# Optimization experiments

Hardware: AMD Instinct MI355X
Metric: run time of the kernel (lower is better)

## Reference

```python
import math
import jax, jax.numpy as jnp
import numpy as np

B, N, HID, NH = 4, 1024, 1024, 16
DH = HID // NH
MLP = int(HID * 4.0)


def _ndense(x, w):
    # NormalizedDense: row-normalize kernel (axis=1 for 2D), alpha=sqrt(w[0].size)=sqrt(out),
    # then divide by sqrt(fan_in).
    norm = jnp.linalg.norm(w, axis=1, keepdims=True)
    alpha = jnp.sqrt(jnp.asarray(w.shape[1], x.dtype))
    wn = w / (norm * alpha + 1e-4)
    wn = wn / jnp.sqrt(jnp.asarray(w.shape[0], x.dtype))
    return x @ wn


def mp_silu(x):
    return jax.nn.silu(x) / 0.596


def pixel_norm(x, eps=1e-4):
    return x * jax.lax.rsqrt(jnp.mean(x * x, axis=-1, keepdims=True) + eps)


def mp_add(a, b, t=0.3):
    return ((1 - t) * a + t * b) / math.sqrt((1 - t) ** 2 + t ** 2)


def setup_inputs() -> dict:
    key = jax.random.key(0)
    ks = jax.random.split(key, 9)
    std = 0.02
    return {
        "x": jax.random.normal(ks[0], (B, N, HID), jnp.float32),
        "c": jax.random.normal(ks[1], (B, HID), jnp.float32),
        "w_cond": std * jax.random.normal(ks[2], (HID, 2 * HID), jnp.float32),
        "w_qkv": std * jax.random.normal(ks[3], (HID, 3 * HID), jnp.float32),
        "w_out": std * jax.random.normal(ks[4], (HID, HID), jnp.float32),
        "w_mlp1": std * jax.random.normal(ks[5], (HID, MLP), jnp.float32),
        "w_mlp2": std * jax.random.normal(ks[6], (MLP, HID), jnp.float32),
        "attn_gain": 0.1 * jax.random.normal(ks[7], (), jnp.float32),
        "mlp_gain": 0.1 * jax.random.normal(ks[8], (), jnp.float32),
    }


def reference(x, c, w_cond, w_qkv, w_out, w_mlp1, w_mlp2, attn_gain, mlp_gain):
    # conditioning -> gain/shift
    cc = mp_silu(c)
    cc = _ndense(cc, w_cond)                       # [B, 2H]
    gain, shift = jnp.split(cc, 2, axis=-1)        # [B, H] each

    # attention branch
    x_cond = pixel_norm(x) * (1 + gain[:, None]) + shift[:, None]
    qkv = _ndense(x_cond, w_qkv)                   # [B, N, 3H]
    q, k, v = jnp.split(qkv, 3, axis=-1)
    q, k, v = pixel_norm(q), pixel_norm(k), pixel_norm(v)

    def split_heads(t):
        return t.reshape(B, N, NH, DH).transpose(0, 2, 1, 3)  # [B, NH, N, DH]

    q, k, v = split_heads(q), split_heads(k), split_heads(v)
    q = q / jnp.sqrt(jnp.sum(q * q, axis=-1, keepdims=True) + 1e-6)
    k = k / jnp.sqrt(jnp.sum(k * k, axis=-1, keepdims=True) + 1e-6)

    attn = jnp.einsum('bhnd,bhmd->bhnm', q, k) / math.sqrt(DH)
    attn = jax.nn.softmax(attn, axis=-1)
    x_attn = jnp.einsum('bhnm,bhmd->bhnd', attn, v)
    x_attn = x_attn.transpose(0, 2, 1, 3).reshape(B, N, HID)
    x_attn = pixel_norm(_ndense(x_attn, w_out)) * jnp.exp(attn_gain)
    x = mp_add(x, x_attn, t=0.3)

    # MLP branch
    x_cond = pixel_norm(x) * (1 + gain[:, None]) + shift[:, None]
    h = mp_silu(pixel_norm(_ndense(x_cond, w_mlp1)))
    x_mlp = pixel_norm(_ndense(h, w_mlp2)) * jnp.exp(mlp_gain)
    x = mp_add(x, x_mlp, t=0.3)
    return x
```

## Files before the change

### kernel.cpp

```cpp
#include <hip/hip_runtime.h>

typedef __bf16 bf16_t;
typedef __attribute__((ext_vector_type(8))) __bf16 bh8;
typedef __attribute__((ext_vector_type(4))) __bf16 bh4;
typedef __attribute__((ext_vector_type(4))) float f32x4;

#define DEV static __device__ __forceinline__

typedef __attribute__((address_space(3))) void lds_void;
typedef const __attribute__((address_space(1))) void glb_void;

DEV void async16(const bf16_t* g, bf16_t* l) {
  __builtin_amdgcn_global_load_lds((glb_void*)g, (lds_void*)l, 16, 0, 0);
}

#define GBAR() asm volatile("s_barrier" ::: "memory")
#define VMW(n) asm volatile("s_waitcnt vmcnt(" #n ")" ::: "memory")

DEV f32x4 mfma16(bh8 a, bh8 b, f32x4 c) {
  return __builtin_amdgcn_mfma_f32_16x16x32_bf16(a, b, c, 0, 0, 0);
}

DEV const bf16_t* lds7(const bf16_t* base, int row, int c) {
  return base + row * 64 + ((c ^ (row & 7)) << 3);
}
DEV bf16_t* ldsP(bf16_t* base, int row, int c) {
  int m = (row & 7) ^ ((row >> 3) & 1);
  return base + row * 64 + ((c ^ m) << 3);
}

DEV float wave_sum(float v) {
#pragma unroll
  for (int m = 32; m > 0; m >>= 1) v += __shfl_xor(v, m, 64);
  return v;
}

DEV float block_sum(float v, float* sbuf) {
  v = wave_sum(v);
  int wid = threadIdx.x >> 6;
  if ((threadIdx.x & 63) == 0) sbuf[wid] = v;
  __syncthreads();
  float r = sbuf[0] + sbuf[1] + sbuf[2] + sbuf[3];
  __syncthreads();
  return r;
}

__global__ void k_wnorm_all(const float* __restrict__ w_cond, const float* __restrict__ w_qkv,
                            const float* __restrict__ w_out, const float* __restrict__ w_mlp1,
                            const float* __restrict__ w_mlp2, float* __restrict__ s) {
  __shared__ float sbuf[4];
  int id = blockIdx.x;
  const float* W; int N, K, row;
  if (id < 1024)      { W = w_cond; N = 2048; K = 1024; row = id; }
  else if (id < 2048) { W = w_qkv;  N = 3072; K = 1024; row = id - 1024; }
  else if (id < 3072) { W = w_out;  N = 1024; K = 1024; row = id - 2048; }
  else if (id < 4096) { W = w_mlp1; N = 4096; K = 1024; row = id - 3072; }
  else                { W = w_mlp2; N = 1024; K = 4096; row = id - 4096; }
  const float4* wr = (const float4*)(W + (size_t)row * N);
  float acc = 0.f;
  for (int i = threadIdx.x; i < (N >> 2); i += 256) {
    float4 w = wr[i];
    acc += w.x*w.x + w.y*w.y + w.z*w.z + w.w*w.w;
  }
  float tot = block_sum(acc, sbuf);
  if (threadIdx.x == 0) {
    float norm = sqrtf(tot);
    s[id] = 1.0f / ((norm * sqrtf((float)N) + 1e-4f) * sqrtf((float)K));
  }
}

__global__ void k_wtrans_all(const float* __restrict__ w_cond, const float* __restrict__ w_qkv,
                             const float* __restrict__ w_out, const float* __restrict__ w_mlp1,
                             const float* __restrict__ w_mlp2, const float* __restrict__ sall,
                             bf16_t* __restrict__ wt_cond, bf16_t* __restrict__ wt_qkv,
                             bf16_t* __restrict__ wt_out, bf16_t* __restrict__ wt_mlp1,
                             bf16_t* __restrict__ wt_mlp2) {
  __shared__ float tile[64][65];
  int id = blockIdx.x;
  const float* W; const float* s; bf16_t* Wt; int K, N, n0, k0;
  if (id < 512)       { W=w_cond; s=sall;      Wt=wt_cond; K=1024; N=2048; int l=id;      n0=(l&31)*64; k0=(l>>5)*64; }
  else if (id < 1280) { W=w_qkv;  s=sall+1024; Wt=wt_qkv;  K=1024; N=3072; int l=id-512;  n0=(l%48)*64; k0=(l/48)*64; }
  else if (id < 1536) { W=w_out;  s=sall+2048; Wt=wt_out;  K=1024; N=1024; int l=id-1280; n0=(l&15)*64; k0=(l>>4)*64; }
  else if (id < 2560) { W=w_mlp1; s=sall+3072; Wt=wt_mlp1; K=1024; N=4096; int l=id-1536; n0=(l&63)*64; k0=(l>>6)*64; }
  else                { W=w_mlp2; s=sall+4096; Wt=wt_mlp2; K=4096; N=1024; int l=id-2560; n0=(l&15)*64; k0=(l>>4)*64; }
  int t = threadIdx.x;
#pragma unroll
  for (int i = t; i < 1024; i += 256) {
    int r = i >> 4, c4 = (i & 15) << 2;
    float sc = s[k0 + r];
    float4 w = *(const float4*)(W + (size_t)(k0 + r) * N + n0 + c4);
    tile[r][c4 + 0] = w.x * sc;
    tile[r][c4 + 1] = w.y * sc;
    tile[r][c4 + 2] = w.z * sc;
    tile[r][c4 + 3] = w.w * sc;
  }
  __syncthreads();
#pragma unroll
  for (int i = t; i < 1024; i += 256) {
    int rr = i >> 4, cc = (i & 15) << 2;
    bh4 o;
    o[0] = (bf16_t)tile[cc + 0][rr];
    o[1] = (bf16_t)tile[cc + 1][rr];
    o[2] = (bf16_t)tile[cc + 2][rr];
    o[3] = (bf16_t)tile[cc + 3][rr];
    *(bh4*)(Wt + (size_t)(n0 + rr) * K + k0 + cc) = o;
  }
}

__global__ void k_cond(const float* __restrict__ c, const bf16_t* __restrict__ wt,
                       float* __restrict__ gs) {
  __shared__ float cc[4][1024];
  int t = threadIdx.x;
  for (int i = t; i < 4096; i += 256) {
    int b = i >> 10, col = i & 1023;
    float x = c[b * 1024 + col];
    float sig = 1.f / (1.f + __expf(-x));
    cc[b][col] = x * sig * (1.f / 0.596f);
  }
  __syncthreads();
  int wid = t >> 6, lane = t & 63;
  int j = blockIdx.x * 4 + wid;
  const bf16_t* wr = wt + (size_t)j * 1024;
  float acc0 = 0, acc1 = 0, acc2 = 0, acc3 = 0;
  for (int i = lane; i < 1024; i += 64) {
    float w = (float)wr[i];
    acc0 += cc[0][i] * w; acc1 += cc[1][i] * w;
    acc2 += cc[2][i] * w; acc3 += cc[3][i] * w;
  }
  float v0 = wave_sum(acc0), v1 = wave_sum(acc1), v2 = wave_sum(acc2), v3 = wave_sum(acc3);
  if (lane == 0) {
    gs[0 * 2048 + j] = v0; gs[1 * 2048 + j] = v1;
    gs[2 * 2048 + j] = v2; gs[3 * 2048 + j] = v3;
  }
}

__global__ void k_xcond(const float* __restrict__ x, const float* __restrict__ gs,
                        bf16_t* __restrict__ xc) {
  __shared__ float sbuf[4];
  int row = blockIdx.x, b = row >> 10, t = threadIdx.x;
  float4 v = ((const float4*)(x + (size_t)row * 1024))[t];
  float ss = v.x*v.x + v.y*v.y + v.z*v.z + v.w*v.w;
  float tot = block_sum(ss, sbuf);
  float r = rsqrtf(tot * (1.f/1024.f) + 1e-4f);
  float4 g  = ((const float4*)(gs + b * 2048))[t];
  float4 sh = ((const float4*)(gs + b * 2048 + 1024))[t];
  bh4 o;
  o[0] = (bf16_t)(v.x * r * (1.f + g.x) + sh.x);
  o[1] = (bf16_t)(v.y * r * (1.f + g.y) + sh.y);
  o[2] = (bf16_t)(v.z * r * (1.f + g.z) + sh.z);
  o[3] = (bf16_t)(v.w * r * (1.f + g.w) + sh.w);
  *(bh4*)(xc + (size_t)row * 1024 + t * 4) = o;
}

__global__ __launch_bounds__(512, 2) void k_gemm8(const bf16_t* __restrict__ A,
                                                  const bf16_t* __restrict__ Bt,
                                                  bf16_t* __restrict__ C,
                                                  int M, int N, int K, int klen) {
  __shared__ __attribute__((aligned(16))) bf16_t As[2][2][256][32];
  __shared__ __attribute__((aligned(16))) bf16_t Bs[2][2][256][32];
  const int ntn = gridDim.x;
  const unsigned flat = blockIdx.x + ntn * blockIdx.y;
  const unsigned q = (ntn * gridDim.y) >> 3;
  const unsigned wg = (flat & 7) * q + (flat >> 3);
  const int m0 = (int)(wg / (unsigned)ntn) * 256;
  const int n0 = (int)(wg % (unsigned)ntn) * 256;
  const size_t kbeg = (size_t)blockIdx.z * klen;
  C += (size_t)blockIdx.z * M * N;
  const int t = threadIdx.x, lane = t & 63;
  const int wm = (t >> 6) >> 2, wn = (t >> 6) & 3;
  const int l15 = lane & 15, quad = lane >> 4;
  const int q8 = (quad ^ ((l15 >> 2) & 2)) * 8;
  const int rA = wm * 128 + l15;
  const int rB = wn * 64 + l15;
  const int sr = t >> 2;
  const int sc = ((t & 3) << 3) ^ ((t & 32) >> 1);
  const int swv = (t >> 6) * 512;
  const bf16_t* AgS = A + (size_t)(m0 + sr) * K + kbeg + sc;
  const bf16_t* BgS = Bt + (size_t)(n0 + sr) * K + kbeg + sc;
  const size_t rstep = (size_t)128 * K;
  const int NT = klen >> 6;
  f32x4 acc[8][4] = {};

#define STG_A(kt_, h_, bb_) { const bf16_t* g = AgS + (kt_) * 64 + (h_) * 32; \
    bf16_t* l = &As[bb_][h_][0][0] + swv; async16(g, l); async16(g + rstep, l + 4096); }
#define STG_B(kt_, h_, bb_) { const bf16_t* g = BgS + (kt_) * 64 + (h_) * 32; \
    bf16_t* l = &Bs[bb_][h_][0][0] + swv; async16(g, l); async16(g + rstep, l + 4096); }

  STG_B(0, 0, 0); STG_B(0, 1, 0);
  STG_A(0, 0, 0); STG_A(0, 1, 0);
  if (NT > 1) { STG_B(1, 0, 1); STG_B(1, 1, 1); VMW(4); } else { VMW(0); }
  GBAR();

  for (int kt = 0; kt < NT; ++kt) {
    const int bb = kt & 1;
    bh8 a[4][2], b[4][2];
#pragma unroll
    for (int m = 0; m < 4; ++m)
#pragma unroll
      for (int kc = 0; kc < 2; ++kc)
        a[m][kc] = *(const bh8*)&As[bb][kc][rA + m * 16][q8];
#pragma unroll
    for (int n = 0; n < 2; ++n)
#pragma unroll
      for (int kc = 0; kc < 2; ++kc)
        b[n][kc] = *(const bh8*)&Bs[bb][kc][rB + n * 16][q8];
    if (kt + 1 < NT) STG_A(kt + 1, 0, bb ^ 1);
    GBAR();
    __builtin_amdgcn_s_setprio(1);
#pragma unroll
    for (int m = 0; m < 4; ++m)
#pragma unroll
      for (int n = 0; n < 2; ++n)
#pragma unroll
        for (int kc = 0; kc < 2; ++kc)
          acc[m][n] = mfma16(a[m][kc], b[n][kc], acc[m][n]);
    __builtin_amdgcn_s_setprio(0);
    GBAR();
#pragma unroll
    for (int n = 0; n < 2; ++n)
#pragma unroll
      for (int kc = 0; kc < 2; ++kc)
        b[2 + n][kc] = *(const bh8*)&Bs[bb][kc][rB + (2 + n) * 16][q8];
    if (kt + 1 < NT) STG_A(kt + 1, 1, bb ^ 1);
    GBAR();
    __builtin_amdgcn_s_setprio(1);
#pragma unroll
    for (int m = 0; m < 4; ++m)
#pragma unroll
      for (int n = 0; n < 2; ++n)
#pragma unroll
        for (int kc = 0; kc < 2; ++kc)
          acc[m][2 + n] = mfma16(a[m][kc], b[2 + n][kc], acc[m][2 + n]);
    __builtin_amdgcn_s_setprio(0);
    GBAR();
#pragma unroll
    for (int m = 0; m < 4; ++m)
#pragma unroll
      for (int kc = 0; kc < 2; ++kc)
        a[m][kc] = *(const bh8*)&As[bb][kc][rA + 64 + m * 16][q8];
    if (kt + 2 < NT) STG_B(kt + 2, 0, bb);
    GBAR();
    __builtin_amdgcn_s_setprio(1);
#pragma unroll
    for (int m = 0; m < 4; ++m)
#pragma unroll
      for (int n = 0; n < 2; ++n)
#pragma unroll
        for (int kc = 0; kc < 2; ++kc)
          acc[4 + m][n] = mfma16(a[m][kc], b[n][kc], acc[4 + m][n]);
    __builtin_amdgcn_s_setprio(0);
    GBAR();
    if (kt + 2 < NT) STG_B(kt + 2, 1, bb);
    __builtin_amdgcn_s_setprio(1);
#pragma unroll
    for (int m = 0; m < 4; ++m)
#pragma unroll
      for (int n = 0; n < 2; ++n)
#pragma unroll
        for (int kc = 0; kc < 2; ++kc)
          acc[4 + m][2 + n] = mfma16(a[m][kc], b[2 + n][kc], acc[4 + m][2 + n]);
    __builtin_amdgcn_s_setprio(0);
    if (kt + 2 < NT) { VMW(4); } else { VMW(0); }
    GBAR();
  }
#undef STG_A
#undef STG_B

  const int cm = m0 + wm * 128 + quad * 4;
  const int cn = n0 + wn * 64 + l15;
#pragma unroll
  for (int m = 0; m < 8; ++m)
#pragma unroll
    for (int n = 0; n < 4; ++n)
#pragma unroll
      for (int r2 = 0; r2 < 4; ++r2)
        C[(size_t)(cm + m * 16 + r2) * N + cn + n * 16] = (bf16_t)acc[m][n][r2];
}

__global__ __launch_bounds__(256, 2) void k_gemm2ph(const bf16_t* __restrict__ A,
                                                    const bf16_t* __restrict__ Bt,
                                                    bf16_t* __restrict__ C,
                                                    int M, int N, int K) {
  __shared__ __attribute__((aligned(16))) bf16_t As[2][2][128][32];
  __shared__ __attribute__((aligned(16))) bf16_t Bs[2][2][128][32];
  const int ntn = gridDim.x;
  const unsigned flat = blockIdx.x + ntn * blockIdx.y;
  const unsigned q = (ntn * gridDim.y) >> 3;
  const unsigned wg = (flat & 7) * q + (flat >> 3);
  const int m0 = (int)(wg / (unsigned)ntn) * 128;
  const int n0 = (int)(wg % (unsigned)ntn) * 128;
  const int t = threadIdx.x, lane = t & 63;
  const int wm = (t >> 6) >> 1, wn = (t >> 6) & 1;
  const int l15 = lane & 15, quad = lane >> 4;
  const int q8 = (quad ^ ((l15 >> 2) & 2)) * 8;
  const int rA = wm * 64 + l15;
  const int rB = wn * 64 + l15;
  const int sr = t >> 2;
  const int sc = ((t & 3) << 3) ^ ((t & 32) >> 1);
  const int swv = (t >> 6) * 512;
  const bf16_t* AgS = A + (size_t)(m0 + sr) * K + sc;
  const bf16_t* BgS = Bt + (size_t)(n0 + sr) * K + sc;
  const size_t rstep = (size_t)64 * K;
  const int NT = K >> 6;
  f32x4 acc[4][4] = {};

#define STG_A(kt_, h_, bb_) { const bf16_t* g = AgS + (kt_) * 64 + (h_) * 32; \
    bf16_t* l = &As[bb_][h_][0][0] + swv; async16(g, l); async16(g + rstep, l + 2048); }
#define STG_B(kt_, h_, bb_) { const bf16_t* g = BgS + (kt_) * 64 + (h_) * 32; \
    bf16_t* l = &Bs[bb_][h_][0][0] + swv; async16(g, l); async16(g + rstep, l + 2048); }

  STG_B(0, 0, 0); STG_B(0, 1, 0);
  STG_A(0, 0, 0); STG_A(0, 1, 0);
  if (NT > 1) { STG_B(1, 0, 1); STG_B(1, 1, 1); VMW(4); } else { VMW(0); }
  GBAR();

  for (int kt = 0; kt < NT; ++kt) {
    const int bb = kt & 1;
    bh8 a[4][2], b[4][2];
#pragma unroll
    for (int m = 0; m < 4; ++m)
#pragma unroll
      for (int kc = 0; kc < 2; ++kc)
        a[m][kc] = *(const bh8*)&As[bb][kc][rA + m * 16][q8];
#pragma unroll
    for (int n = 0; n < 4; ++n)
#pragma unroll
      for (int kc = 0; kc < 2; ++kc)
        b[n][kc] = *(const bh8*)&Bs[bb][kc][rB + n * 16][q8];
    if (kt + 1 < NT) { STG_A(kt + 1, 0, bb ^ 1); STG_A(kt + 1, 1, bb ^ 1); }
    GBAR();
    __builtin_amdgcn_s_setprio(1);
#pragma unroll
    for (int m = 0; m < 4; ++m)
#pragma unroll
      for (int n = 0; n < 2; ++n)
#pragma unroll
        for (int kc = 0; kc < 2; ++kc)
          acc[m][n] = mfma16(a[m][kc], b[n][kc], acc[m][n]);
    __builtin_amdgcn_s_setprio(0);
    GBAR();
    if (kt + 2 < NT) { STG_B(kt + 2, 0, bb); STG_B(kt + 2, 1, bb); }
    __builtin_amdgcn_s_setprio(1);
#pragma unroll
    for (int m = 0; m < 4; ++m)
#pragma unroll
      for (int n = 0; n < 2; ++n)
#pragma unroll
        for (int kc = 0; kc < 2; ++kc)
          acc[m][2 + n] = mfma16(a[m][kc], b[2 + n][kc], acc[m][2 + n]);
    __builtin_amdgcn_s_setprio(0);
    if (kt + 2 < NT) { VMW(4); } else { VMW(0); }
    GBAR();
  }
#undef STG_A
#undef STG_B

  const int cm = m0 + wm * 64 + quad * 4;
  const int cn = n0 + wn * 64 + l15;
#pragma unroll
  for (int m = 0; m < 4; ++m)
#pragma unroll
    for (int n = 0; n < 4; ++n)
#pragma unroll
      for (int r2 = 0; r2 < 4; ++r2)
        C[(size_t)(cm + m * 16 + r2) * N + cn + n * 16] = (bf16_t)acc[m][n][r2];
}

__global__ void k_qkvnorm(const bf16_t* __restrict__ qkv, bf16_t* __restrict__ qo,
                          bf16_t* __restrict__ ko, float* __restrict__ rsv) {
  __shared__ float sbuf[4];
  const int row = blockIdx.x, b = row >> 10, n = row & 1023, t = threadIdx.x;
  const bf16_t* rp = qkv + (size_t)row * 3072;
  bh4 q4 = *(const bh4*)(rp + t * 4);
  bh4 k4 = *(const bh4*)(rp + 1024 + t * 4);
  bh4 v4 = *(const bh4*)(rp + 2048 + t * 4);
  float4 q = {(float)q4[0], (float)q4[1], (float)q4[2], (float)q4[3]};
  float4 k = {(float)k4[0], (float)k4[1], (float)k4[2], (float)k4[3]};
  float4 v = {(float)v4[0], (float)v4[1], (float)v4[2], (float)v4[3]};
  float sq = q.x*q.x + q.y*q.y + q.z*q.z + q.w*q.w;
  float sk = k.x*k.x + k.y*k.y + k.z*k.z + k.w*k.w;
  float sv = v.x*v.x + v.y*v.y + v.z*v.z + v.w*v.w;
  float tq = block_sum(sq, sbuf);
  float tk = block_sum(sk, sbuf);
  float tv = block_sum(sv, sbuf);
  float rq = rsqrtf(tq * (1.f/1024.f) + 1e-4f);
  float rk = rsqrtf(tk * (1.f/1024.f) + 1e-4f);
  float rv = rsqrtf(tv * (1.f/1024.f) + 1e-4f);
  float hq = sq, hk = sk;
#pragma unroll
  for (int m = 1; m < 16; m <<= 1) { hq += __shfl_xor(hq, m, 64); hk += __shfl_xor(hk, m, 64); }
  float qs = rq * rsqrtf(rq*rq*hq + 1e-6f);
  float ks = rk * rsqrtf(rk*rk*hk + 1e-6f);
  int h = t >> 4, d = (t & 15) * 4;
  size_t base = ((size_t)(b * 16 + h) * 1024 + n) * 64 + d;
  bh4 oq, okk;
  oq[0]=(bf16_t)(q.x*qs); oq[1]=(bf16_t)(q.y*qs); oq[2]=(bf16_t)(q.z*qs); oq[3]=(bf16_t)(q.w*qs);
  okk[0]=(bf16_t)(k.x*ks); okk[1]=(bf16_t)(k.y*ks); okk[2]=(bf16_t)(k.z*ks); okk[3]=(bf16_t)(k.w*ks);
  *(bh4*)(qo + base) = oq;
  *(bh4*)(ko + base) = okk;
  if (t == 0) rsv[row] = rv;
}

__global__ void k_vtrans(const bf16_t* __restrict__ qkv, const float* __restrict__ rsv,
                         bf16_t* __restrict__ vt) {
  __shared__ bf16_t tile[64][72];
  const int n0 = blockIdx.x * 64, bh = blockIdx.y;
  const int b = bh >> 4, h = bh & 15;
  const int t = threadIdx.x;
  const bf16_t* src = qkv + ((size_t)(b * 1024 + n0)) * 3072 + 2048 + h * 64;
#pragma unroll
  for (int i = t; i < 512; i += 256) {
    int r = i >> 3, p = (i & 7) * 8;
    float sc = rsv[b * 1024 + n0 + r];
    bh8 vv = *(const bh8*)(src + (size_t)r * 3072 + p);
    bh8 o8;
#pragma unroll
    for (int j = 0; j < 8; j++) o8[j] = (bf16_t)((float)vv[j] * sc);
    *(bh8*)&tile[r][p] = o8;
  }
  __syncthreads();
  bf16_t* dst = vt + (size_t)bh * 64 * 1024 + n0;
#pragma unroll
  for (int i = t; i < 512; i += 256) {
    int d = i & 63, nch = (i >> 6) * 8;
    bh8 o;
#pragma unroll
    for (int j = 0; j < 8; j++) o[j] = tile[nch + j][d];
    *(bh8*)(dst + (size_t)d * 1024 + nch) = o;
  }
}

__global__ __launch_bounds__(256, 2) void k_attn(const bf16_t* __restrict__ Q,
                                                 const bf16_t* __restrict__ K,
                                                 const bf16_t* __restrict__ Vt_g,
                                                 bf16_t* __restrict__ O) {
  __shared__ __attribute__((aligned(16))) bf16_t Qs[128][64];
  __shared__ __attribute__((aligned(16))) bf16_t Ks[2][64][64];
  __shared__ __attribute__((aligned(16))) bf16_t Vt[2][64][64];
  __shared__ __attribute__((aligned(16))) bf16_t Ps[128][64];
  const unsigned flat = blockIdx.x + 8u * blockIdx.y;
  const int qt = (int)((flat >> 3) & 7);
  const int bh = (int)((flat & 7) * 8 + (flat >> 6));
  const int b = bh >> 4, h = bh & 15;
  const int t = threadIdx.x, lane = t & 63, wid = t >> 6;
  const int l15 = lane & 15, quad = lane >> 4;
  const int strip = wid * 32;
  const int srow = t >> 3;
  const int scol = ((t & 7) ^ (srow & 7)) << 3;
  const int swv = wid * 512;
  const bf16_t* Qg = Q + ((size_t)bh * 1024 + qt * 128) * 64;
  const bf16_t* Kg = K + (size_t)bh * 1024 * 64;
  const bf16_t* Vg = Vt_g + (size_t)bh * 64 * 1024;

#pragma unroll
  for (int c2 = 0; c2 < 4; ++c2)
    async16(Qg + (size_t)(c2 * 32 + srow) * 64 + scol, &Qs[0][0] + c2 * 2048 + swv);
#pragma unroll
  for (int r0 = 0; r0 < 64; r0 += 32) {
    async16(Kg + (size_t)(r0 + srow) * 64 + scol, &Ks[0][0][0] + r0 * 64 + swv);
    async16(Vg + (size_t)(r0 + srow) * 1024 + scol, &Vt[0][0][0] + r0 * 64 + swv);
  }
  VMW(0);
  GBAR();

  f32x4 o[2][4] = {};
  float rs[2][4] = {{}, {}};
  for (int kt = 0; kt < 16; ++kt) {
    const int bb = kt & 1;
    const int kv0 = kt * 64;
    if (kt < 15) {
#pragma unroll
      for (int r0 = 0; r0 < 64; r0 += 32) {
        async16(Kg + (size_t)(kv0 + 64 + r0 + srow) * 64 + scol,
                &Ks[bb ^ 1][0][0] + r0 * 64 + swv);
        async16(Vg + (size_t)(r0 + srow) * 1024 + kv0 + 64 + scol,
                &Vt[bb ^ 1][0][0] + r0 * 64 + swv);
      }
    }
    f32x4 s[2][4] = {};
    bh8 aq[2][2], bk[4][2];
#pragma unroll
    for (int rf = 0; rf < 2; ++rf)
#pragma unroll
      for (int kc = 0; kc < 2; ++kc)
        aq[rf][kc] = *(const bh8*)lds7(&Qs[0][0], strip + rf * 16 + l15, kc * 4 + quad);
#pragma unroll
    for (int j = 0; j < 4; ++j)
#pragma unroll
      for (int kc = 0; kc < 2; ++kc)
        bk[j][kc] = *(const bh8*)lds7(&Ks[bb][0][0], j * 16 + l15, kc * 4 + quad);
    __builtin_amdgcn_s_setprio(1);
#pragma unroll
    for (int rf = 0; rf < 2; ++rf)
#pragma unroll
      for (int j = 0; j < 4; ++j)
#pragma unroll
        for (int kc = 0; kc < 2; ++kc)
          s[rf][j] = mfma16(aq[rf][kc], bk[j][kc], s[rf][j]);
    __builtin_amdgcn_s_setprio(0);
#pragma unroll
    for (int rf = 0; rf < 2; ++rf)
#pragma unroll
      for (int j = 0; j < 4; ++j)
#pragma unroll
        for (int r = 0; r < 4; ++r) {
          float p = __expf(s[rf][j][r] * 0.125f);
          bf16_t pb = (bf16_t)p;
          rs[rf][r] += (float)pb;
          int prow = strip + rf * 16 + quad * 4 + r;
          ldsP(&Ps[0][0], prow, j * 2 + (l15 >> 3))[l15 & 7] = pb;
        }
    bh8 ap[2][2], bv[4][2];
#pragma unroll
    for (int rf = 0; rf < 2; ++rf)
#pragma unroll
      for (int kc = 0; kc < 2; ++kc)
        ap[rf][kc] = *(const bh8*)ldsP(&Ps[0][0], strip + rf * 16 + l15, kc * 4 + quad);
#pragma unroll
    for (int j = 0; j < 4; ++j)
#pragma unroll
      for (int kc = 0; kc < 2; ++kc)
        bv[j][kc] = *(const bh8*)lds7(&Vt[bb][0][0], j * 16 + l15, kc * 4 + quad);
    __builtin_amdgcn_s_setprio(1);
#pragma unroll
    for (int rf = 0; rf < 2; ++rf)
#pragma unroll
      for (int j = 0; j < 4; ++j)
#pragma unroll
        for (int kc = 0; kc < 2; ++kc)
          o[rf][j] = mfma16(ap[rf][kc], bv[j][kc], o[rf][j]);
    __builtin_amdgcn_s_setprio(0);
    if (kt < 15) { VMW(0); GBAR(); }
  }
#pragma unroll
  for (int rf = 0; rf < 2; ++rf)
#pragma unroll
    for (int r = 0; r < 4; ++r) {
      float v = rs[rf][r];
      v += __shfl_xor(v, 1, 64); v += __shfl_xor(v, 2, 64);
      v += __shfl_xor(v, 4, 64); v += __shfl_xor(v, 8, 64);
      float inv = 1.f / v;
      int n = qt * 128 + strip + rf * 16 + quad * 4 + r;
#pragma unroll
      for (int j = 0; j < 4; ++j)
        O[((size_t)b * 1024 + n) * 1024 + h * 64 + j * 16 + l15] = (bf16_t)(o[rf][j][r] * inv);
    }
}

__global__ void k_amerge(const bf16_t* __restrict__ y, const float* __restrict__ x,
                         const float* __restrict__ gs, const float* __restrict__ again,
                         bf16_t* __restrict__ x1, bf16_t* __restrict__ xc2) {
  __shared__ float sbuf[4];
  int row = blockIdx.x, b = row >> 10, t = threadIdx.x;
  bh4 a = *(const bh4*)(y + (size_t)row * 1024 + t * 4);
  float4 yv = {(float)a[0], (float)a[1], (float)a[2], (float)a[3]};
  float4 xv = ((const float4*)(x + (size_t)row * 1024))[t];
  float ss = yv.x*yv.x + yv.y*yv.y + yv.z*yv.z + yv.w*yv.w;
  float tot = block_sum(ss, sbuf);
  float r = rsqrtf(tot * (1.f/1024.f) + 1e-4f);
  float ag = __expf(again[0]);
  const float C1 = 0.7f / 0.76157731059f, C2 = 0.3f / 0.76157731059f;
  float4 xo;
  xo.x = C1 * xv.x + C2 * (yv.x * r * ag);
  xo.y = C1 * xv.y + C2 * (yv.y * r * ag);
  xo.z = C1 * xv.z + C2 * (yv.z * r * ag);
  xo.w = C1 * xv.w + C2 * (yv.w * r * ag);
  bh4 x1o;
  x1o[0] = (bf16_t)xo.x; x1o[1] = (bf16_t)xo.y; x1o[2] = (bf16_t)xo.z; x1o[3] = (bf16_t)xo.w;
  *(bh4*)(x1 + (size_t)row * 1024 + t * 4) = x1o;
  float ss1 = xo.x*xo.x + xo.y*xo.y + xo.z*xo.z + xo.w*xo.w;
  float tot1 = block_sum(ss1, sbuf);
  float r1 = rsqrtf(tot1 * (1.f/1024.f) + 1e-4f);
  float4 g  = ((const float4*)(gs + b * 2048))[t];
  float4 sh = ((const float4*)(gs + b * 2048 + 1024))[t];
  bh4 o;
  o[0] = (bf16_t)(xo.x * r1 * (1.f + g.x) + sh.x);
  o[1] = (bf16_t)(xo.y * r1 * (1.f + g.y) + sh.y);
  o[2] = (bf16_t)(xo.z * r1 * (1.f + g.z) + sh.z);
  o[3] = (bf16_t)(xo.w * r1 * (1.f + g.w) + sh.w);
  *(bh4*)(xc2 + (size_t)row * 1024 + t * 4) = o;
}

__global__ void k_mlpnorm(const bf16_t* __restrict__ hf, bf16_t* __restrict__ hb) {
  __shared__ float sbuf[4];
  int row = blockIdx.x, t = threadIdx.x;
  const bf16_t* rp = hf + (size_t)row * 4096;
  float4 v[4]; float ss = 0.f;
#pragma unroll
  for (int i = 0; i < 4; i++) {
    bh4 bv = *(const bh4*)(rp + (t + 256 * i) * 4);
    v[i].x = (float)bv[0]; v[i].y = (float)bv[1]; v[i].z = (float)bv[2]; v[i].w = (float)bv[3];
    ss += v[i].x*v[i].x + v[i].y*v[i].y + v[i].z*v[i].z + v[i].w*v[i].w;
  }
  float tot = block_sum(ss, sbuf);
  float r = rsqrtf(tot * (1.f/4096.f) + 1e-4f);
#pragma unroll
  for (int i = 0; i < 4; i++) {
    float a[4] = {v[i].x, v[i].y, v[i].z, v[i].w};
    bh4 o;
#pragma unroll
    for (int j = 0; j < 4; j++) {
      float u = a[j] * r;
      float sig = 1.f / (1.f + __expf(-u));
      o[j] = (bf16_t)(u * sig * (1.f / 0.596f));
    }
    *(bh4*)(hb + (size_t)row * 4096 + (t + 256 * i) * 4) = o;
  }
}

__global__ void k_fmerge(const bf16_t* __restrict__ y, const bf16_t* __restrict__ x1,
                         const float* __restrict__ mgain, float* __restrict__ out) {
  __shared__ float sbuf[4];
  int row = blockIdx.x, t = threadIdx.x;
  const size_t PS = (size_t)4096 * 1024;
  float4 yv = {0.f, 0.f, 0.f, 0.f};
#pragma unroll
  for (int p = 0; p < 4; p++) {
    bh4 yp = *(const bh4*)(y + p * PS + (size_t)row * 1024 + t * 4);
    yv.x += (float)yp[0]; yv.y += (float)yp[1]; yv.z += (float)yp[2]; yv.w += (float)yp[3];
  }
  bh4 xb = *(const bh4*)(x1 + (size_t)row * 1024 + t * 4);
  float4 xv = {(float)xb[0], (float)xb[1], (float)xb[2], (float)xb[3]};
  float ss = yv.x*yv.x + yv.y*yv.y + yv.z*yv.z + yv.w*yv.w;
  float tot = block_sum(ss, sbuf);
  float r = rsqrtf(tot * (1.f/1024.f) + 1e-4f);
  float mg = __expf(mgain[0]);
  const float C1 = 0.7f / 0.76157731059f, C2 = 0.3f / 0.76157731059f;
  float4 o;
  o.x = C1 * xv.x + C2 * (yv.x * r * mg);
  o.y = C1 * xv.y + C2 * (yv.y * r * mg);
  o.z = C1 * xv.z + C2 * (yv.z * r * mg);
  o.w = C1 * xv.w + C2 * (yv.w * r * mg);
  ((float4*)(out + (size_t)row * 1024))[t] = o;
}

extern "C" void kernel_launch(void* const* d_in, const int* in_sizes, int n_in,
                              void* d_out, int out_size, void* d_ws, size_t ws_size,
                              hipStream_t stream) {
  const float* x      = (const float*)d_in[0];
  const float* c      = (const float*)d_in[1];
  const float* w_cond = (const float*)d_in[2];
  const float* w_qkv  = (const float*)d_in[3];
  const float* w_out  = (const float*)d_in[4];
  const float* w_mlp1 = (const float*)d_in[5];
  const float* w_mlp2 = (const float*)d_in[6];
  const float* again  = (const float*)d_in[7];
  const float* mgain  = (const float*)d_in[8];
  float* out = (float*)d_out;
  char* ws = (char*)d_ws;

  bf16_t* wt_cond = (bf16_t*)(ws + 0);
  bf16_t* wt_qkv  = (bf16_t*)(ws + 4194304);
  bf16_t* wt_out  = (bf16_t*)(ws + 10485760);
  bf16_t* wt_mlp1 = (bf16_t*)(ws + 12582912);
  bf16_t* wt_mlp2 = (bf16_t*)(ws + 20971520);
  float*  sn      = (float*)(ws + 29360128);
  float*  gs      = (float*)(ws + 29392896);
  bf16_t* xc      = (bf16_t*)(ws + 29425664);
  bf16_t* qh      = (bf16_t*)(ws + 37814272);
  bf16_t* kh      = (bf16_t*)(ws + 46202880);
  float*  rsv     = (float*)(ws + 54591488);
  bf16_t* xattn   = (bf16_t*)(ws + 62980096);
  bf16_t* hb      = (bf16_t*)(ws + 37814272);
  bf16_t* x1      = (bf16_t*)(ws + 71368704);
  bf16_t* vt      = (bf16_t*)(ws + 79757312);
  bf16_t* buf_b   = (bf16_t*)(ws + 88145920);

  k_wnorm_all<<<8192, 256, 0, stream>>>(w_cond, w_qkv, w_out, w_mlp1, w_mlp2, sn);
  k_wtrans_all<<<3584, 256, 0, stream>>>(w_cond, w_qkv, w_out, w_mlp1, w_mlp2, sn,
                                         wt_cond, wt_qkv, wt_out, wt_mlp1, wt_mlp2);

  k_cond<<<512, 256, 0, stream>>>(c, wt_cond, gs);
  k_xcond<<<4096, 256, 0, stream>>>(x, gs, xc);
  k_gemm8<<<dim3(12, 16, 1), 512, 0, stream>>>(xc, wt_qkv, buf_b, 4096, 3072, 1024, 1024);
  k_qkvnorm<<<4096, 256, 0, stream>>>(buf_b, qh, kh, rsv);
  k_vtrans<<<dim3(16, 64), 256, 0, stream>>>(buf_b, rsv, vt);
  k_attn<<<dim3(8, 64), 256, 0, stream>>>(qh, kh, vt, xattn);
  k_gemm2ph<<<dim3(8, 32), 256, 0, stream>>>(xattn, wt_out, buf_b, 4096, 1024, 1024);
  k_amerge<<<4096, 256, 0, stream>>>(buf_b, x, gs, again, x1, xc);
  k_gemm8<<<dim3(16, 16, 1), 512, 0, stream>>>(xc, wt_mlp1, buf_b, 4096, 4096, 1024, 1024);
  k_mlpnorm<<<4096, 256, 0, stream>>>(buf_b, hb);
  k_gemm8<<<dim3(4, 16, 4), 512, 0, stream>>>(hb, wt_mlp2, buf_b, 4096, 1024, 4096, 1024);
  k_fmerge<<<4096, 256, 0, stream>>>(buf_b, x1, mgain, out);
  (void)in_sizes; (void)n_in; (void)out_size; (void)ws_size;
}
```

Measured before the change: 352.9 us.

## Fuse weight row-norm into transpose pass and fold scales into activations

Removes the separate weight-norm kernel, which read every weight matrix a second time. Sum-of-squares is now accumulated with atomics inside the transpose kernel, then finalized by a tiny kernel. The per-row scale is applied to the GEMM input activations (cond, xcond, attention output, amerge, mlpnorm) instead of being baked into the transposed weights. This adds two small launches, atomic traffic and slightly different bf16 rounding.

```diff
diff --git a/kernel.cpp b/kernel.cpp
--- a/kernel.cpp
+++ b/kernel.cpp
@@ -45,54 +45,37 @@
   return r;
 }
 
-__global__ void k_wnorm_all(const float* __restrict__ w_cond, const float* __restrict__ w_qkv,
-                            const float* __restrict__ w_out, const float* __restrict__ w_mlp1,
-                            const float* __restrict__ w_mlp2, float* __restrict__ s) {
-  __shared__ float sbuf[4];
-  int id = blockIdx.x;
-  const float* W; int N, K, row;
-  if (id < 1024)      { W = w_cond; N = 2048; K = 1024; row = id; }
-  else if (id < 2048) { W = w_qkv;  N = 3072; K = 1024; row = id - 1024; }
-  else if (id < 3072) { W = w_out;  N = 1024; K = 1024; row = id - 2048; }
-  else if (id < 4096) { W = w_mlp1; N = 4096; K = 1024; row = id - 3072; }
-  else                { W = w_mlp2; N = 1024; K = 4096; row = id - 4096; }
-  const float4* wr = (const float4*)(W + (size_t)row * N);
-  float acc = 0.f;
-  for (int i = threadIdx.x; i < (N >> 2); i += 256) {
-    float4 w = wr[i];
-    acc += w.x*w.x + w.y*w.y + w.z*w.z + w.w*w.w;
-  }
-  float tot = block_sum(acc, sbuf);
-  if (threadIdx.x == 0) {
-    float norm = sqrtf(tot);
-    s[id] = 1.0f / ((norm * sqrtf((float)N) + 1e-4f) * sqrtf((float)K));
-  }
+__global__ void k_zero(float* __restrict__ p) {
+  p[blockIdx.x * 256 + threadIdx.x] = 0.f;
 }
 
 __global__ void k_wtrans_all(const float* __restrict__ w_cond, const float* __restrict__ w_qkv,
                              const float* __restrict__ w_out, const float* __restrict__ w_mlp1,
-                             const float* __restrict__ w_mlp2, const float* __restrict__ sall,
+                             const float* __restrict__ w_mlp2, float* __restrict__ ssq,
                              bf16_t* __restrict__ wt_cond, bf16_t* __restrict__ wt_qkv,
                              bf16_t* __restrict__ wt_out, bf16_t* __restrict__ wt_mlp1,
                              bf16_t* __restrict__ wt_mlp2) {
   __shared__ float tile[64][65];
   int id = blockIdx.x;
-  const float* W; const float* s; bf16_t* Wt; int K, N, n0, k0;
-  if (id < 512)       { W=w_cond; s=sall;      Wt=wt_cond; K=1024; N=2048; int l=id;      n0=(l&31)*64; k0=(l>>5)*64; }
-  else if (id < 1280) { W=w_qkv;  s=sall+1024; Wt=wt_qkv;  K=1024; N=3072; int l=id-512;  n0=(l%48)*64; k0=(l/48)*64; }
-  else if (id < 1536) { W=w_out;  s=sall+2048; Wt=wt_out;  K=1024; N=1024; int l=id-1280; n0=(l&15)*64; k0=(l>>4)*64; }
-  else if (id < 2560) { W=w_mlp1; s=sall+3072; Wt=wt_mlp1; K=1024; N=4096; int l=id-1536; n0=(l&63)*64; k0=(l>>6)*64; }
-  else                { W=w_mlp2; s=sall+4096; Wt=wt_mlp2; K=4096; N=1024; int l=id-2560; n0=(l&15)*64; k0=(l>>4)*64; }
+  const float* W; bf16_t* Wt; int K, N, n0, k0, sb;
+  if (id < 512)       { W=w_cond; Wt=wt_cond; K=1024; N=2048; sb=0;    int l=id;      n0=(l&31)*64; k0=(l>>5)*64; }
+  else if (id < 1280) { W=w_qkv;  Wt=wt_qkv;  K=1024; N=3072; sb=1024; int l=id-512;  n0=(l%48)*64; k0=(l/48)*64; }
+  else if (id < 1536) { W=w_out;  Wt=wt_out;  K=1024; N=1024; sb=2048; int l=id-1280; n0=(l&15)*64; k0=(l>>4)*64; }
+  else if (id < 2560) { W=w_mlp1; Wt=wt_mlp1; K=1024; N=4096; sb=3072; int l=id-1536; n0=(l&63)*64; k0=(l>>6)*64; }
+  else                { W=w_mlp2; Wt=wt_mlp2; K=4096; N=1024; sb=4096; int l=id-2560; n0=(l&15)*64; k0=(l>>4)*64; }
   int t = threadIdx.x;
 #pragma unroll
   for (int i = t; i < 1024; i += 256) {
     int r = i >> 4, c4 = (i & 15) << 2;
-    float sc = s[k0 + r];
     float4 w = *(const float4*)(W + (size_t)(k0 + r) * N + n0 + c4);
-    tile[r][c4 + 0] = w.x * sc;
-    tile[r][c4 + 1] = w.y * sc;
-    tile[r][c4 + 2] = w.z * sc;
-    tile[r][c4 + 3] = w.w * sc;
+    tile[r][c4 + 0] = w.x;
+    tile[r][c4 + 1] = w.y;
+    tile[r][c4 + 2] = w.z;
+    tile[r][c4 + 3] = w.w;
+    float ss = w.x*w.x + w.y*w.y + w.z*w.z + w.w*w.w;
+#pragma unroll
+    for (int m = 1; m < 16; m <<= 1) ss += __shfl_xor(ss, m, 64);
+    if ((t & 15) == 0) atomicAdd(&ssq[sb + k0 + r], ss);
   }
   __syncthreads();
 #pragma unroll
@@ -107,15 +90,27 @@
   }
 }
 
+__global__ void k_sfin(const float* __restrict__ ssq, float* __restrict__ s) {
+  int id = blockIdx.x * 256 + threadIdx.x;
+  int N, K;
+  if (id < 1024)      { N = 2048; K = 1024; }
+  else if (id < 2048) { N = 3072; K = 1024; }
+  else if (id < 3072) { N = 1024; K = 1024; }
+  else if (id < 4096) { N = 4096; K = 1024; }
+  else                { N = 1024; K = 4096; }
+  float norm = sqrtf(ssq[id]);
+  s[id] = 1.0f / ((norm * sqrtf((float)N) + 1e-4f) * sqrtf((float)K));
+}
+
 __global__ void k_cond(const float* __restrict__ c, const bf16_t* __restrict__ wt,
-                       float* __restrict__ gs) {
+                       const float* __restrict__ sc, float* __restrict__ gs) {
   __shared__ float cc[4][1024];
   int t = threadIdx.x;
   for (int i = t; i < 4096; i += 256) {
     int b = i >> 10, col = i & 1023;
     float x = c[b * 1024 + col];
     float sig = 1.f / (1.f + __expf(-x));
-    cc[b][col] = x * sig * (1.f / 0.596f);
+    cc[b][col] = x * sig * (1.f / 0.596f) * sc[col];
   }
   __syncthreads();
   int wid = t >> 6, lane = t & 63;
@@ -135,7 +130,7 @@
 }
 
 __global__ void k_xcond(const float* __restrict__ x, const float* __restrict__ gs,
-                        bf16_t* __restrict__ xc) {
+                        const float* __restrict__ sq, bf16_t* __restrict__ xc) {
   __shared__ float sbuf[4];
   int row = blockIdx.x, b = row >> 10, t = threadIdx.x;
   float4 v = ((const float4*)(x + (size_t)row * 1024))[t];
@@ -144,11 +139,12 @@
   float r = rsqrtf(tot * (1.f/1024.f) + 1e-4f);
   float4 g  = ((const float4*)(gs + b * 2048))[t];
   float4 sh = ((const float4*)(gs + b * 2048 + 1024))[t];
+  float4 sv = ((const float4*)sq)[t];
   bh4 o;
-  o[0] = (bf16_t)(v.x * r * (1.f + g.x) + sh.x);
-  o[1] = (bf16_t)(v.y * r * (1.f + g.y) + sh.y);
-  o[2] = (bf16_t)(v.z * r * (1.f + g.z) + sh.z);
-  o[3] = (bf16_t)(v.w * r * (1.f + g.w) + sh.w);
+  o[0] = (bf16_t)((v.x * r * (1.f + g.x) + sh.x) * sv.x);
+  o[1] = (bf16_t)((v.y * r * (1.f + g.y) + sh.y) * sv.y);
+  o[2] = (bf16_t)((v.z * r * (1.f + g.z) + sh.z) * sv.z);
+  o[3] = (bf16_t)((v.w * r * (1.f + g.w) + sh.w) * sv.w);
   *(bh4*)(xc + (size_t)row * 1024 + t * 4) = o;
 }
 
@@ -433,6 +429,7 @@
 __global__ __launch_bounds__(256, 2) void k_attn(const bf16_t* __restrict__ Q,
                                                  const bf16_t* __restrict__ K,
                                                  const bf16_t* __restrict__ Vt_g,
+                                                 const float* __restrict__ so,
                                                  bf16_t* __restrict__ O) {
   __shared__ __attribute__((aligned(16))) bf16_t Qs[128][64];
   __shared__ __attribute__((aligned(16))) bf16_t Ks[2][64][64];
@@ -532,6 +529,9 @@
     __builtin_amdgcn_s_setprio(0);
     if (kt < 15) { VMW(0); GBAR(); }
   }
+  float soj[4];
+#pragma unroll
+  for (int j = 0; j < 4; ++j) soj[j] = so[h * 64 + j * 16 + l15];
 #pragma unroll
   for (int rf = 0; rf < 2; ++rf)
 #pragma unroll
@@ -543,12 +543,14 @@
       int n = qt * 128 + strip + rf * 16 + quad * 4 + r;
 #pragma unroll
       for (int j = 0; j < 4; ++j)
-        O[((size_t)b * 1024 + n) * 1024 + h * 64 + j * 16 + l15] = (bf16_t)(o[rf][j][r] * inv);
+        O[((size_t)b * 1024 + n) * 1024 + h * 64 + j * 16 + l15] =
+            (bf16_t)(o[rf][j][r] * inv * soj[j]);
     }
 }
 
 __global__ void k_amerge(const bf16_t* __restrict__ y, const float* __restrict__ x,
                          const float* __restrict__ gs, const float* __restrict__ again,
+                         const float* __restrict__ sm1,
                          bf16_t* __restrict__ x1, bf16_t* __restrict__ xc2) {
   __shared__ float sbuf[4];
   int row = blockIdx.x, b = row >> 10, t = threadIdx.x;
@@ -573,15 +575,17 @@
   float r1 = rsqrtf(tot1 * (1.f/1024.f) + 1e-4f);
   float4 g  = ((const float4*)(gs + b * 2048))[t];
   float4 sh = ((const float4*)(gs + b * 2048 + 1024))[t];
+  float4 sv = ((const float4*)sm1)[t];
   bh4 o;
-  o[0] = (bf16_t)(xo.x * r1 * (1.f + g.x) + sh.x);
-  o[1] = (bf16_t)(xo.y * r1 * (1.f + g.y) + sh.y);
-  o[2] = (bf16_t)(xo.z * r1 * (1.f + g.z) + sh.z);
-  o[3] = (bf16_t)(xo.w * r1 * (1.f + g.w) + sh.w);
+  o[0] = (bf16_t)((xo.x * r1 * (1.f + g.x) + sh.x) * sv.x);
+  o[1] = (bf16_t)((xo.y * r1 * (1.f + g.y) + sh.y) * sv.y);
+  o[2] = (bf16_t)((xo.z * r1 * (1.f + g.z) + sh.z) * sv.z);
+  o[3] = (bf16_t)((xo.w * r1 * (1.f + g.w) + sh.w) * sv.w);
   *(bh4*)(xc2 + (size_t)row * 1024 + t * 4) = o;
 }
 
-__global__ void k_mlpnorm(const bf16_t* __restrict__ hf, bf16_t* __restrict__ hb) {
+__global__ void k_mlpnorm(const bf16_t* __restrict__ hf, const float* __restrict__ sm2,
+                          bf16_t* __restrict__ hb) {
   __shared__ float sbuf[4];
   int row = blockIdx.x, t = threadIdx.x;
   const bf16_t* rp = hf + (size_t)row * 4096;
@@ -597,12 +601,14 @@
 #pragma unroll
   for (int i = 0; i < 4; i++) {
     float a[4] = {v[i].x, v[i].y, v[i].z, v[i].w};
+    float4 s4 = ((const float4*)sm2)[t + 256 * i];
+    float sa[4] = {s4.x, s4.y, s4.z, s4.w};
     bh4 o;
 #pragma unroll
     for (int j = 0; j < 4; j++) {
       float u = a[j] * r;
       float sig = 1.f / (1.f + __expf(-u));
-      o[j] = (bf16_t)(u * sig * (1.f / 0.596f));
+      o[j] = (bf16_t)(u * sig * (1.f / 0.596f) * sa[j]);
     }
     *(bh4*)(hb + (size_t)row * 4096 + (t + 256 * i) * 4) = o;
   }
@@ -665,21 +671,23 @@
   bf16_t* x1      = (bf16_t*)(ws + 71368704);
   bf16_t* vt      = (bf16_t*)(ws + 79757312);
   bf16_t* buf_b   = (bf16_t*)(ws + 88145920);
-
-  k_wnorm_all<<<8192, 256, 0, stream>>>(w_cond, w_qkv, w_out, w_mlp1, w_mlp2, sn);
-  k_wtrans_all<<<3584, 256, 0, stream>>>(w_cond, w_qkv, w_out, w_mlp1, w_mlp2, sn,
+  float*  ssq     = gs;
+
+  k_zero<<<32, 256, 0, stream>>>(ssq);
+  k_wtrans_all<<<3584, 256, 0, stream>>>(w_cond, w_qkv, w_out, w_mlp1, w_mlp2, ssq,
                                          wt_cond, wt_qkv, wt_out, wt_mlp1, wt_mlp2);
-
-  k_cond<<<512, 256, 0, stream>>>(c, wt_cond, gs);
-  k_xcond<<<4096, 256, 0, stream>>>(x, gs, xc);
+  k_sfin<<<32, 256, 0, stream>>>(ssq, sn);
+
+  k_cond<<<512, 256, 0, stream>>>(c, wt_cond, sn, gs);
+  k_xcond<<<4096, 256, 0, stream>>>(x, gs, sn + 1024, xc);
   k_gemm8<<<dim3(12, 16, 1), 512, 0, stream>>>(xc, wt_qkv, buf_b, 4096, 3072, 1024, 1024);
   k_qkvnorm<<<4096, 256, 0, stream>>>(buf_b, qh, kh, rsv);
   k_vtrans<<<dim3(16, 64), 256, 0, stream>>>(buf_b, rsv, vt);
-  k_attn<<<dim3(8, 64), 256, 0, stream>>>(qh, kh, vt, xattn);
+  k_attn<<<dim3(8, 64), 256, 0, stream>>>(qh, kh, vt, sn + 2048, xattn);
   k_gemm2ph<<<dim3(8, 32), 256, 0, stream>>>(xattn, wt_out, buf_b, 4096, 1024, 1024);
-  k_amerge<<<4096, 256, 0, stream>>>(buf_b, x, gs, again, x1, xc);
+  k_amerge<<<4096, 256, 0, stream>>>(buf_b, x, gs, again, sn + 3072, x1, xc);
   k_gemm8<<<dim3(16, 16, 1), 512, 0, stream>>>(xc, wt_mlp1, buf_b, 4096, 4096, 1024, 1024);
-  k_mlpnorm<<<4096, 256, 0, stream>>>(buf_b, hb);
+  k_mlpnorm<<<4096, 256, 0, stream>>>(buf_b, sn + 4096, hb);
   k_gemm8<<<dim3(4, 16, 4), 512, 0, stream>>>(hb, wt_mlp2, buf_b, 4096, 1024, 4096, 1024);
   k_fmerge<<<4096, 256, 0, stream>>>(buf_b, x1, mgain, out);
   (void)in_sizes; (void)n_in; (void)out_size; (void)ws_size;
```

New measurement: 352.5 us. No clear change (-0.1%).
